# Optimization experiments

Hardware: AMD Instinct MI355X
Metric: run time of the kernel (lower is better)

The kernel has to match this reference:

```python
import jax, jax.numpy as jnp
import numpy as np

N_AGENTS = 32
STATE_DIM = 2048
EMBED = 64
BS, T = 64, 32


def setup_inputs() -> dict:
    key = jax.random.key(0)
    ks = jax.random.split(key, 12)
    def lin(k, fan_in, fan_out):
        return jax.random.normal(k, (fan_in, fan_out), dtype=jnp.float32) / np.sqrt(fan_in)
    return {
        "agent_qs": jax.random.normal(ks[0], (BS, T, N_AGENTS), dtype=jnp.float32),
        "states": jax.random.normal(ks[1], (BS, T, STATE_DIM), dtype=jnp.float32),
        "Ww1": lin(ks[2], STATE_DIM, EMBED * N_AGENTS),
        "bw1": jnp.zeros((EMBED * N_AGENTS,), jnp.float32),
        "Wwf": lin(ks[3], STATE_DIM, EMBED),
        "bwf": jnp.zeros((EMBED,), jnp.float32),
        "Wb1": lin(ks[4], STATE_DIM, EMBED),
        "bb1": jnp.zeros((EMBED,), jnp.float32),
        "Wv1": lin(ks[5], STATE_DIM, EMBED),
        "bv1": jnp.zeros((EMBED,), jnp.float32),
        "Wv2": lin(ks[6], EMBED, 1),
        "bv2": jnp.zeros((1,), jnp.float32),
    }


def _mix(qs, st, Ww1, bw1, Wwf, bwf, Wb1, bb1, Wv1, bv1, Wv2, bv2):
    # qs: [B,1,A], st: [B,S] -> q_tot [B]
    w1 = jnp.abs(st @ Ww1 + bw1).reshape(-1, N_AGENTS, EMBED)          # [B,A,E]
    b1 = (st @ Wb1 + bb1)[:, None, :]                                   # [B,1,E]
    hidden = jax.nn.elu(jnp.einsum('bia,bae->bie', qs, w1) + b1)        # [B,1,E]
    w_final = jnp.abs(st @ Wwf + bwf)                                   # [B,E]
    v = jax.nn.relu(st @ Wv1 + bv1) @ Wv2 + bv2                         # [B,1]
    y = jnp.einsum('bie,be->bi', hidden, w_final) + v                   # [B,1]
    return y[:, 0]


def reference(agent_qs, states, Ww1, bw1, Wwf, bwf, Wb1, bb1, Wv1, bv1, Wv2, bv2):
    bs = agent_qs.shape[0]
    st = states.reshape(-1, STATE_DIM)                   # [B,S]
    qs = agent_qs.reshape(-1, 1, N_AGENTS)               # [B,1,A]
    B = st.shape[0]
    params = (Ww1, bw1, Wwf, bwf, Wb1, bb1, Wv1, bv1, Wv2, bv2)

    # --- wc_calculate (fully detached) ---
    q_tot = _mix(qs, st, *params)                        # [B]
    dim2 = STATE_DIM // N_AGENTS
    st3 = st.reshape(B, N_AGENTS, dim2)
    mask = 1.0 - jnp.eye(N_AGENTS, dtype=st.dtype)       # [A,A]: row i zeros agent-i chunk
    masked = (st3[None, :, :, :] * mask[:, None, :, None]).reshape(N_AGENTS * B, STATE_DIM)
    qs_rep = jnp.broadcast_to(qs[None], (N_AGENTS, B, 1, N_AGENTS)).reshape(N_AGENTS * B, 1, N_AGENTS)
    q1 = _mix(qs_rep, masked, *params).reshape(N_AGENTS, B)
    wc = jnp.abs(q_tot[None, :] - q1).T                  # [B,A]
    wc = wc / jnp.maximum(jnp.linalg.norm(wc, axis=1, keepdims=True), 1e-12)
    wc = jax.lax.stop_gradient(wc)[:, None, :]           # [B,1,A]

    # --- final mix with importance-weighted qs ---
    q_tot_final = _mix(qs * wc, st, *params)             # [B]
    return q_tot_final.reshape(bs, -1, 1)
```

## Files before the change

### kernel.cpp

```cpp
#include <hip/hip_runtime.h>
#include <math.h>
#include <stdint.h>

#define NA 32
#define SD 2048
#define BT 2048
#define NFRG 144

typedef float floatx4 __attribute__((ext_vector_type(4)));
typedef short bf16x8  __attribute__((ext_vector_type(8)));

__device__ __forceinline__ unsigned short f2bf(float f) {
    union { float f; uint32_t u; } v; v.f = f;
    uint32_t r = v.u + 0x7FFFu + ((v.u >> 16) & 1u);
    return (unsigned short)(r >> 16);
}


__global__ __launch_bounds__(256) void k0_ast(const float* __restrict__ st,
                                              unsigned short* __restrict__ stA) {
    int idx = blockIdx.x * 256 + threadIdx.x;
    int m = idx >> 8, kg = idx & 255;
    int k0 = kg * 8;
    const float* src = st + (size_t)m * SD + k0;
    float4 v0 = *(const float4*)src;
    float4 v1 = *(const float4*)(src + 4);
    int bt = m >> 4, l16 = m & 15, kc = kg >> 2, quad = kg & 3;
    unsigned short* dst = stA + ((size_t)bt * 64 + kc) * 512 + (quad * 16 + l16) * 8;
    ushort4 o0, o1;
    o0.x = f2bf(v0.x); o0.y = f2bf(v0.y); o0.z = f2bf(v0.z); o0.w = f2bf(v0.w);
    o1.x = f2bf(v1.x); o1.y = f2bf(v1.y); o1.z = f2bf(v1.z); o1.w = f2bf(v1.w);
    *(ushort4*)(dst)     = o0;
    *(ushort4*)(dst + 4) = o1;
}

__global__ __launch_bounds__(256) void k0_wswz(const float* __restrict__ Ww1,
                                               const float* __restrict__ Wwf,
                                               const float* __restrict__ Wb1,
                                               const float* __restrict__ Wv1,
                                               unsigned short* __restrict__ Wswz) {
    __shared__ float tile[32][33];
    const int n0 = blockIdx.x * 32;
    const int k0 = blockIdx.y * 32;
    const float* src; int ld = 64, nb = 0;
    if (n0 < 2048)      { src = Ww1; ld = 2048; nb = n0; }
    else if (n0 < 2112) { src = Wwf; nb = n0 - 2048; }
    else if (n0 < 2176) { src = Wb1; nb = n0 - 2112; }
    else if (n0 < 2240) { src = Wv1; nb = n0 - 2176; }
    else                { src = nullptr; }
    const int t = threadIdx.x;
    {
        int nl = t & 31, kl0 = t >> 5;
        #pragma unroll
        for (int r = 0; r < 4; r++) {
            int kl = kl0 + r * 8;
            tile[kl][nl] = src ? src[(size_t)(k0 + kl) * ld + nb + nl] : 0.f;
        }
    }
    __syncthreads();
    {
        int kl = t & 31, nl0 = t >> 5;
        #pragma unroll
        for (int r = 0; r < 4; r++) {
            int nl = nl0 + r * 8;
            int n = n0 + nl, k = k0 + kl;
            int f = n >> 4, l16 = n & 15;
            int i = k >> 6, kr = k & 63;
            int h = kr >> 5, quad = (kr & 31) >> 3, j = kr & 7;
            size_t off = (((size_t)i * NFRG + f) * 2 + h) * 512 + (quad * 16 + l16) * 8 + j;
            Wswz[off] = f2bf(tile[kl][nl]);
        }
    }
}

__global__ void k0_bias(const float* __restrict__ bw1, const float* __restrict__ bwf,
                        const float* __restrict__ bb1, const float* __restrict__ bv1,
                        float* __restrict__ bcat) {
    int n = blockIdx.x * 256 + threadIdx.x;
    if (n >= NFRG * 16) return;
    float v = 0.f;
    if (n < 2048)      v = bw1[n];
    else if (n < 2112) v = bwf[n - 2048];
    else if (n < 2176) v = bb1[n - 2112];
    else if (n < 2240) v = bv1[n - 2176];
    bcat[n] = v;
}

__global__ __launch_bounds__(256) void k1_gemm(const unsigned short* __restrict__ stA,
                                               const unsigned short* __restrict__ Wswz,
                                               const float* __restrict__ bcat,
                                               float* __restrict__ Ycn)
{
    const int t = threadIdx.x;
    const int m0t = blockIdx.x * 4;
    const int n0f = blockIdx.y * 8;
    const int wid = t >> 6, lane = t & 63;
    const int wm = wid & 1, wn = wid >> 1;
    const int l16 = lane & 15;

    floatx4 acc[2][4];
    #pragma unroll
    for (int i = 0; i < 2; i++)
        #pragma unroll
        for (int j = 0; j < 4; j++) acc[i][j] = (floatx4)0.f;

    const unsigned short* Ap0 = stA + ((size_t)(m0t + wm * 2 + 0) * 64) * 512 + lane * 8;
    const unsigned short* Ap1 = stA + ((size_t)(m0t + wm * 2 + 1) * 64) * 512 + lane * 8;

    #pragma unroll 2
    for (int kc = 0; kc < 64; kc++) {
        bf16x8 a0 = *(const bf16x8*)(Ap0 + (size_t)kc * 512);
        bf16x8 a1 = *(const bf16x8*)(Ap1 + (size_t)kc * 512);
        const int i = kc >> 1, h = kc & 1;
        const unsigned short* Bp =
            Wswz + (((size_t)i * NFRG + n0f + wn * 4) * 2 + h) * 512 + lane * 8;
        #pragma unroll
        for (int nf = 0; nf < 4; nf++) {
            bf16x8 b = *(const bf16x8*)(Bp + (size_t)nf * 1024);
            acc[0][nf] = __builtin_amdgcn_mfma_f32_16x16x32_bf16(a0, b, acc[0][nf], 0, 0, 0);
            acc[1][nf] = __builtin_amdgcn_mfma_f32_16x16x32_bf16(a1, b, acc[1][nf], 0, 0, 0);
        }
    }

    #pragma unroll
    for (int mf = 0; mf < 2; mf++)
        #pragma unroll
        for (int nf = 0; nf < 4; nf++) {
            const int f  = n0f + wn * 4 + nf;
            const int bt = m0t + wm * 2 + mf;
            const float bias = bcat[f * 16 + l16];
            floatx4 o;
            #pragma unroll
            for (int r = 0; r < 4; r++) o[r] = -(acc[mf][nf][r] + bias);
            *(floatx4*)(Ycn + ((size_t)bt * NFRG + f) * 256 + lane * 4) = o;
        }
}

__global__ __launch_bounds__(64) void k3_q1(
    const unsigned short* __restrict__ stA, const float* __restrict__ qs,
    const unsigned short* __restrict__ Wswz, const float* __restrict__ Wv2,
    const float* __restrict__ bv2, const float* __restrict__ Ycn,
    float* __restrict__ q1)
{
    const int bt = blockIdx.x;
    const int i  = blockIdx.y;
    __shared__ float qs_s[16][33];

    const int t = threadIdx.x;
    const int quad = t >> 4, l16 = t & 15;

    {
        int b = t >> 2, a0 = (t & 3) * 8;
        const float* src = qs + (size_t)(bt * 16 + b) * NA + a0;
        #pragma unroll
        for (int u = 0; u < 8; u++) qs_s[b][a0 + u] = src[u];
    }
    bf16x8 A0 = *(const bf16x8*)(stA + ((size_t)bt * 64 + 2 * i + 0) * 512 + t * 8);
    bf16x8 A1 = *(const bf16x8*)(stA + ((size_t)bt * 64 + 2 * i + 1) * 512 + t * 8);
    __syncthreads();

    floatx4 hid[4];
    #pragma unroll
    for (int nf = 0; nf < 4; nf++) hid[nf] = (floatx4)0.f;

    const float*          Yb = Ycn  + (size_t)bt * NFRG * 256;
    const unsigned short* Wb = Wswz + (size_t)i * NFRG * 1024;

    for (int a = 0; a < 32; a++) {
        const float*          yp = Yb + (size_t)(a * 4) * 256 + t * 4;
        const unsigned short* wp = Wb + (size_t)(a * 4) * 1024 + t * 8;
        floatx4 acc[4];
        #pragma unroll
        for (int nf = 0; nf < 4; nf++) acc[nf] = *(const floatx4*)(yp + nf * 256);
        #pragma unroll
        for (int nf = 0; nf < 4; nf++) {
            bf16x8 b0 = *(const bf16x8*)(wp + nf * 1024);
            bf16x8 b1 = *(const bf16x8*)(wp + nf * 1024 + 512);
            acc[nf] = __builtin_amdgcn_mfma_f32_16x16x32_bf16(A0, b0, acc[nf], 0, 0, 0);
            acc[nf] = __builtin_amdgcn_mfma_f32_16x16x32_bf16(A1, b1, acc[nf], 0, 0, 0);
        }
        float qv[4];
        #pragma unroll
        for (int r = 0; r < 4; r++) qv[r] = qs_s[quad * 4 + r][a];
        #pragma unroll
        for (int nf = 0; nf < 4; nf++)
            #pragma unroll
            for (int r = 0; r < 4; r++)
                hid[nf][r] += qv[r] * fabsf(acc[nf][r]);
    }

    floatx4 wff[4], b1f[4], vacc = (floatx4)0.f;
    #pragma unroll
    for (int nft = 0; nft < 12; nft++) {
        const int f = 128 + nft;
        floatx4 c = *(const floatx4*)(Yb + (size_t)f * 256 + t * 4);
        const unsigned short* wp = Wb + (size_t)f * 1024 + t * 8;
        c = __builtin_amdgcn_mfma_f32_16x16x32_bf16(A0, *(const bf16x8*)(wp),       c, 0, 0, 0);
        c = __builtin_amdgcn_mfma_f32_16x16x32_bf16(A1, *(const bf16x8*)(wp + 512), c, 0, 0, 0);
        if (nft < 4) {
            #pragma unroll
            for (int r = 0; r < 4; r++) wff[nft][r] = fabsf(c[r]);
        } else if (nft < 8) {
            #pragma unroll
            for (int r = 0; r < 4; r++) b1f[nft - 4][r] = -c[r];
        } else {
            float wv2 = Wv2[(nft - 8) * 16 + l16];
            #pragma unroll
            for (int r = 0; r < 4; r++) vacc[r] += fmaxf(-c[r], 0.f) * wv2;
        }
    }

    const float bv2v = bv2[0];
    #pragma unroll
    for (int r = 0; r < 4; r++) {
        float s = vacc[r];
        #pragma unroll
        for (int nf = 0; nf < 4; nf++) {
            float h = hid[nf][r] + b1f[nf][r];
            h = h > 0.f ? h : expm1f(h);
            s += h * wff[nf][r];
        }
        s += __shfl_xor(s, 1); s += __shfl_xor(s, 2);
        s += __shfl_xor(s, 4); s += __shfl_xor(s, 8);
        if (l16 == 0) q1[(size_t)i * BT + bt * 16 + quad * 4 + r] = s + bv2v;
    }
}

__global__ __launch_bounds__(256) void k4_final(
    const float* __restrict__ qs, const float* __restrict__ Ycn,
    const float* __restrict__ q1, const float* __restrict__ Wv2,
    const float* __restrict__ bv2, float* __restrict__ out)
{
    const int bt = blockIdx.x;
    __shared__ float qs_s[16][33];
    __shared__ float qw_s[16][33];
    __shared__ float hidp[4][16][64];
    __shared__ float wfb[16][64], b1b[16][64], vb[16][64];
    __shared__ float qt[16];

    const int t = threadIdx.x, w = t >> 6, lane = t & 63;
    const int quad = lane >> 4, l16 = lane & 15;
    const float bv2v = bv2[0];

    {
        int l = t * 2;
        float2 v = *(const float2*)&qs[(size_t)(bt * 16 + (l >> 5)) * NA + (l & 31)];
        qs_s[l >> 5][(l & 31) + 0] = v.x;
        qs_s[l >> 5][(l & 31) + 1] = v.y;
    }
    __syncthreads();

    const float* Yb = Ycn + (size_t)bt * NFRG * 256;

    floatx4 hid[4];
    #pragma unroll
    for (int nf = 0; nf < 4; nf++) hid[nf] = (floatx4)0.f;
    for (int ia = 0; ia < 8; ia++) {
        const int a = w * 8 + ia;
        const float* yp = Yb + (size_t)(a * 4) * 256 + lane * 4;
        float qv[4];
        #pragma unroll
        for (int r = 0; r < 4; r++) qv[r] = qs_s[quad * 4 + r][a];
        #pragma unroll
        for (int nf = 0; nf < 4; nf++) {
            floatx4 c = *(const floatx4*)(yp + nf * 256);
            #pragma unroll
            for (int r = 0; r < 4; r++) hid[nf][r] += qv[r] * fabsf(c[r]);
        }
    }
    #pragma unroll
    for (int nf = 0; nf < 4; nf++)
        #pragma unroll
        for (int r = 0; r < 4; r++)
            hidp[w][quad * 4 + r][nf * 16 + l16] = hid[nf][r];

    #pragma unroll
    for (int fi = 0; fi < 3; fi++) {
        const int nft = w * 3 + fi;
        floatx4 c = *(const floatx4*)(Yb + (size_t)(128 + nft) * 256 + lane * 4);
        const int e = (nft & 3) * 16 + l16;
        #pragma unroll
        for (int r = 0; r < 4; r++) {
            int b = quad * 4 + r;
            if (nft < 4)      wfb[b][e] = fabsf(c[r]);
            else if (nft < 8) b1b[b][e] = -c[r];
            else              vb[b][e]  = fmaxf(-c[r], 0.f) * Wv2[e];
        }
    }
    __syncthreads();

    #pragma unroll
    for (int bb = 0; bb < 4; bb++) {
        int b = w * 4 + bb;
        float h = hidp[0][b][lane] + hidp[1][b][lane]
                + hidp[2][b][lane] + hidp[3][b][lane] + b1b[b][lane];
        h = h > 0.f ? h : expm1f(h);
        float val = h * wfb[b][lane] + vb[b][lane];
        #pragma unroll
        for (int off = 32; off > 0; off >>= 1) val += __shfl_xor(val, off);
        if (lane == 0) qt[b] = val + bv2v;
    }
    __syncthreads();

    {
        const int rr = w * 4 + quad;
        float qtv = qt[rr];
        float d0 = fabsf(qtv - q1[(size_t)(2 * l16 + 0) * BT + bt * 16 + rr]);
        float d1 = fabsf(qtv - q1[(size_t)(2 * l16 + 1) * BT + bt * 16 + rr]);
        float ss = d0 * d0 + d1 * d1;
        ss += __shfl_xor(ss, 1); ss += __shfl_xor(ss, 2);
        ss += __shfl_xor(ss, 4); ss += __shfl_xor(ss, 8);
        float inv = 1.f / fmaxf(sqrtf(ss), 1e-12f);
        qw_s[rr][2 * l16 + 0] = qs_s[rr][2 * l16 + 0] * d0 * inv;
        qw_s[rr][2 * l16 + 1] = qs_s[rr][2 * l16 + 1] * d1 * inv;
    }
    __syncthreads();

    floatx4 hid2[4];
    #pragma unroll
    for (int nf = 0; nf < 4; nf++) hid2[nf] = (floatx4)0.f;
    for (int ia = 0; ia < 8; ia++) {
        const int a = w * 8 + ia;
        const float* yp = Yb + (size_t)(a * 4) * 256 + lane * 4;
        float qv[4];
        #pragma unroll
        for (int r = 0; r < 4; r++) qv[r] = qw_s[quad * 4 + r][a];
        #pragma unroll
        for (int nf = 0; nf < 4; nf++) {
            floatx4 c = *(const floatx4*)(yp + nf * 256);
            #pragma unroll
            for (int r = 0; r < 4; r++) hid2[nf][r] += qv[r] * fabsf(c[r]);
        }
    }
    #pragma unroll
    for (int nf = 0; nf < 4; nf++)
        #pragma unroll
        for (int r = 0; r < 4; r++)
            hidp[w][quad * 4 + r][nf * 16 + l16] = hid2[nf][r];
    __syncthreads();

    #pragma unroll
    for (int bb = 0; bb < 4; bb++) {
        int b = w * 4 + bb;
        float h = hidp[0][b][lane] + hidp[1][b][lane]
                + hidp[2][b][lane] + hidp[3][b][lane] + b1b[b][lane];
        h = h > 0.f ? h : expm1f(h);
        float val = h * wfb[b][lane] + vb[b][lane];
        #pragma unroll
        for (int off = 32; off > 0; off >>= 1) val += __shfl_xor(val, off);
        if (lane == 0) out[bt * 16 + b] = val + bv2v;
    }
}

extern "C" void kernel_launch(void* const* d_in, const int* in_sizes, int n_in,
                              void* d_out, int out_size, void* d_ws, size_t ws_size,
                              hipStream_t stream) {
    const float* qs  = (const float*)d_in[0];
    const float* st  = (const float*)d_in[1];
    const float* Ww1 = (const float*)d_in[2];
    const float* bw1 = (const float*)d_in[3];
    const float* Wwf = (const float*)d_in[4];
    const float* bwf = (const float*)d_in[5];
    const float* Wb1 = (const float*)d_in[6];
    const float* bb1 = (const float*)d_in[7];
    const float* Wv1 = (const float*)d_in[8];
    const float* bv1 = (const float*)d_in[9];
    const float* Wv2 = (const float*)d_in[10];
    const float* bv2 = (const float*)d_in[11];
    float* out = (float*)d_out;

    float* Ycn           = (float*)d_ws;
    unsigned short* stA  = (unsigned short*)(Ycn + (size_t)128 * NFRG * 256);
    unsigned short* Wswz = stA + (size_t)SD * SD;
    float* bcat          = (float*)(Wswz + (size_t)32 * NFRG * 1024);
    float* q1v           = bcat + NFRG * 16;

    k0_ast <<<(SD * SD / 8 + 255) / 256, 256, 0, stream>>>(st, stA);
    k0_wswz<<<dim3(NFRG / 2, SD / 32), 256, 0, stream>>>(Ww1, Wwf, Wb1, Wv1, Wswz);
    k0_bias<<<(NFRG * 16 + 255) / 256, 256, 0, stream>>>(bw1, bwf, bb1, bv1, bcat);

    k1_gemm<<<dim3(BT / 64, NFRG / 8), 256, 0, stream>>>(stA, Wswz, bcat, Ycn);
    k3_q1  <<<dim3(BT / 16, NA), 64, 0, stream>>>(stA, qs, Wswz, Wv2, bv2, Ycn, q1v);
    k4_final<<<BT / 16, 256, 0, stream>>>(qs, Ycn, q1v, Wv2, bv2, out);
}
```

Baseline: 217.9 us.

## Store GEMM output in bf16, prefetch GEMM operands, remap repacking kernels

The intermediate projection Ycn is now stored as bf16 instead of fp32. This halves the traffic for the GEMM epilogue and for the reads in the q1 and final kernels, at the cost of extra rounding in values that later feed differences between mixes. The GEMM main loop now register double-buffers the A and B fragments to hide load latency. The state and weight repacking kernels are remapped so that each thread writes a contiguous 8-element fragment directly, and the weight repack drops its shared-memory transpose in favor of strided global reads.

```diff
diff --git a/kernel.cpp b/kernel.cpp
--- a/kernel.cpp
+++ b/kernel.cpp
@@ -16,20 +16,31 @@
     return (unsigned short)(r >> 16);
 }
 
+__device__ __forceinline__ floatx4 bf4_to_f4(ushort4 u) {
+    union { uint32_t i; float f; } t;
+    floatx4 r;
+    t.i = (uint32_t)u.x << 16; r[0] = t.f;
+    t.i = (uint32_t)u.y << 16; r[1] = t.f;
+    t.i = (uint32_t)u.z << 16; r[2] = t.f;
+    t.i = (uint32_t)u.w << 16; r[3] = t.f;
+    return r;
+}
+
 
 __global__ __launch_bounds__(256) void k0_ast(const float* __restrict__ st,
                                               unsigned short* __restrict__ stA) {
-    int idx = blockIdx.x * 256 + threadIdx.x;
-    int m = idx >> 8, kg = idx & 255;
-    int k0 = kg * 8;
-    const float* src = st + (size_t)m * SD + k0;
-    float4 v0 = *(const float4*)src;
+    const int t  = threadIdx.x;
+    const int kc = blockIdx.x * 4 + (t >> 6);
+    const int bt = blockIdx.y;
+    const int l  = t & 63;
+    const int quad = l >> 4, l16 = l & 15;
+    const float* src = st + (size_t)(bt * 16 + l16) * SD + kc * 32 + quad * 8;
+    float4 v0 = *(const float4*)(src);
     float4 v1 = *(const float4*)(src + 4);
-    int bt = m >> 4, l16 = m & 15, kc = kg >> 2, quad = kg & 3;
-    unsigned short* dst = stA + ((size_t)bt * 64 + kc) * 512 + (quad * 16 + l16) * 8;
     ushort4 o0, o1;
     o0.x = f2bf(v0.x); o0.y = f2bf(v0.y); o0.z = f2bf(v0.z); o0.w = f2bf(v0.w);
     o1.x = f2bf(v1.x); o1.y = f2bf(v1.y); o1.z = f2bf(v1.z); o1.w = f2bf(v1.w);
+    unsigned short* dst = stA + ((size_t)bt * 64 + kc) * 512 + l * 8;
     *(ushort4*)(dst)     = o0;
     *(ushort4*)(dst + 4) = o1;
 }
@@ -39,38 +50,32 @@
                                                const float* __restrict__ Wb1,
                                                const float* __restrict__ Wv1,
                                                unsigned short* __restrict__ Wswz) {
-    __shared__ float tile[32][33];
-    const int n0 = blockIdx.x * 32;
-    const int k0 = blockIdx.y * 32;
-    const float* src; int ld = 64, nb = 0;
-    if (n0 < 2048)      { src = Ww1; ld = 2048; nb = n0; }
-    else if (n0 < 2112) { src = Wwf; nb = n0 - 2048; }
-    else if (n0 < 2176) { src = Wb1; nb = n0 - 2112; }
-    else if (n0 < 2240) { src = Wv1; nb = n0 - 2176; }
-    else                { src = nullptr; }
     const int t = threadIdx.x;
-    {
-        int nl = t & 31, kl0 = t >> 5;
-        #pragma unroll
-        for (int r = 0; r < 4; r++) {
-            int kl = kl0 + r * 8;
-            tile[kl][nl] = src ? src[(size_t)(k0 + kl) * ld + nb + nl] : 0.f;
-        }
-    }
-    __syncthreads();
-    {
-        int kl = t & 31, nl0 = t >> 5;
-        #pragma unroll
-        for (int r = 0; r < 4; r++) {
-            int nl = nl0 + r * 8;
-            int n = n0 + nl, k = k0 + kl;
-            int f = n >> 4, l16 = n & 15;
-            int i = k >> 6, kr = k & 63;
-            int h = kr >> 5, quad = (kr & 31) >> 3, j = kr & 7;
-            size_t off = (((size_t)i * NFRG + f) * 2 + h) * 512 + (quad * 16 + l16) * 8 + j;
-            Wswz[off] = f2bf(tile[kl][nl]);
-        }
-    }
+    const int i = blockIdx.y;
+    const int f = blockIdx.x * 2 + (t >> 7);
+    const int h = (t >> 6) & 1;
+    const int l = t & 63;
+    const int quad = l >> 4, l16 = l & 15;
+    const int n = f * 16 + l16;
+
+    const float* src; int ld, nr = 0;
+    if (f < 128)      { src = Ww1; ld = 2048; nr = n; }
+    else if (f < 132) { src = Wwf; ld = 64;   nr = n - 2048; }
+    else if (f < 136) { src = Wb1; ld = 64;   nr = n - 2112; }
+    else if (f < 140) { src = Wv1; ld = 64;   nr = n - 2176; }
+    else              { src = nullptr; ld = 64; }
+
+    const int k0 = i * 64 + h * 32 + quad * 8;
+    unsigned short vals[8];
+    #pragma unroll
+    for (int j = 0; j < 8; j++)
+        vals[j] = src ? f2bf(src[(size_t)(k0 + j) * ld + nr]) : (unsigned short)0;
+
+    unsigned short* dst = Wswz + (((size_t)i * NFRG + f) * 2 + h) * 512 + l * 8;
+    ushort4 o0 = {vals[0], vals[1], vals[2], vals[3]};
+    ushort4 o1 = {vals[4], vals[5], vals[6], vals[7]};
+    *(ushort4*)(dst)     = o0;
+    *(ushort4*)(dst + 4) = o1;
 }
 
 __global__ void k0_bias(const float* __restrict__ bw1, const float* __restrict__ bwf,
@@ -89,7 +94,7 @@
 __global__ __launch_bounds__(256) void k1_gemm(const unsigned short* __restrict__ stA,
                                                const unsigned short* __restrict__ Wswz,
                                                const float* __restrict__ bcat,
-                                               float* __restrict__ Ycn)
+                                               unsigned short* __restrict__ Ycn)
 {
     const int t = threadIdx.x;
     const int m0t = blockIdx.x * 4;
@@ -106,20 +111,35 @@
 
     const unsigned short* Ap0 = stA + ((size_t)(m0t + wm * 2 + 0) * 64) * 512 + lane * 8;
     const unsigned short* Ap1 = stA + ((size_t)(m0t + wm * 2 + 1) * 64) * 512 + lane * 8;
-
-    #pragma unroll 2
+    const unsigned short* Bbase = Wswz + ((size_t)(n0f + wn * 4) * 2) * 512 + lane * 8;
+
+    bf16x8 a0c = *(const bf16x8*)(Ap0);
+    bf16x8 a1c = *(const bf16x8*)(Ap1);
+    bf16x8 bc[4];
+    #pragma unroll
+    for (int nf = 0; nf < 4; nf++)
+        bc[nf] = *(const bf16x8*)(Bbase + (size_t)nf * 1024);
+
     for (int kc = 0; kc < 64; kc++) {
-        bf16x8 a0 = *(const bf16x8*)(Ap0 + (size_t)kc * 512);
-        bf16x8 a1 = *(const bf16x8*)(Ap1 + (size_t)kc * 512);
-        const int i = kc >> 1, h = kc & 1;
-        const unsigned short* Bp =
-            Wswz + (((size_t)i * NFRG + n0f + wn * 4) * 2 + h) * 512 + lane * 8;
-        #pragma unroll
-        for (int nf = 0; nf < 4; nf++) {
-            bf16x8 b = *(const bf16x8*)(Bp + (size_t)nf * 1024);
-            acc[0][nf] = __builtin_amdgcn_mfma_f32_16x16x32_bf16(a0, b, acc[0][nf], 0, 0, 0);
-            acc[1][nf] = __builtin_amdgcn_mfma_f32_16x16x32_bf16(a1, b, acc[1][nf], 0, 0, 0);
-        }
+        bf16x8 a0n, a1n, bn[4];
+        if (kc < 63) {
+            const int kn = kc + 1;
+            a0n = *(const bf16x8*)(Ap0 + (size_t)kn * 512);
+            a1n = *(const bf16x8*)(Ap1 + (size_t)kn * 512);
+            const unsigned short* Bp =
+                Bbase + ((size_t)(kn >> 1) * NFRG * 2 + (kn & 1)) * 512;
+            #pragma unroll
+            for (int nf = 0; nf < 4; nf++)
+                bn[nf] = *(const bf16x8*)(Bp + (size_t)nf * 1024);
+        }
+        #pragma unroll
+        for (int nf = 0; nf < 4; nf++) {
+            acc[0][nf] = __builtin_amdgcn_mfma_f32_16x16x32_bf16(a0c, bc[nf], acc[0][nf], 0, 0, 0);
+            acc[1][nf] = __builtin_amdgcn_mfma_f32_16x16x32_bf16(a1c, bc[nf], acc[1][nf], 0, 0, 0);
+        }
+        a0c = a0n; a1c = a1n;
+        #pragma unroll
+        for (int nf = 0; nf < 4; nf++) bc[nf] = bn[nf];
     }
 
     #pragma unroll
@@ -129,17 +149,19 @@
             const int f  = n0f + wn * 4 + nf;
             const int bt = m0t + wm * 2 + mf;
             const float bias = bcat[f * 16 + l16];
-            floatx4 o;
-            #pragma unroll
-            for (int r = 0; r < 4; r++) o[r] = -(acc[mf][nf][r] + bias);
-            *(floatx4*)(Ycn + ((size_t)bt * NFRG + f) * 256 + lane * 4) = o;
+            ushort4 o;
+            o.x = f2bf(-(acc[mf][nf][0] + bias));
+            o.y = f2bf(-(acc[mf][nf][1] + bias));
+            o.z = f2bf(-(acc[mf][nf][2] + bias));
+            o.w = f2bf(-(acc[mf][nf][3] + bias));
+            *(ushort4*)(Ycn + ((size_t)bt * NFRG + f) * 256 + lane * 4) = o;
         }
 }
 
 __global__ __launch_bounds__(64) void k3_q1(
     const unsigned short* __restrict__ stA, const float* __restrict__ qs,
     const unsigned short* __restrict__ Wswz, const float* __restrict__ Wv2,
-    const float* __restrict__ bv2, const float* __restrict__ Ycn,
+    const float* __restrict__ bv2, const unsigned short* __restrict__ Ycn,
     float* __restrict__ q1)
 {
     const int bt = blockIdx.x;
@@ -163,15 +185,16 @@
     #pragma unroll
     for (int nf = 0; nf < 4; nf++) hid[nf] = (floatx4)0.f;
 
-    const float*          Yb = Ycn  + (size_t)bt * NFRG * 256;
+    const unsigned short* Yb = Ycn  + (size_t)bt * NFRG * 256;
     const unsigned short* Wb = Wswz + (size_t)i * NFRG * 1024;
 
     for (int a = 0; a < 32; a++) {
-        const float*          yp = Yb + (size_t)(a * 4) * 256 + t * 4;
+        const unsigned short* yp = Yb + (size_t)(a * 4) * 256 + t * 4;
         const unsigned short* wp = Wb + (size_t)(a * 4) * 1024 + t * 8;
         floatx4 acc[4];
         #pragma unroll
-        for (int nf = 0; nf < 4; nf++) acc[nf] = *(const floatx4*)(yp + nf * 256);
+        for (int nf = 0; nf < 4; nf++)
+            acc[nf] = bf4_to_f4(*(const ushort4*)(yp + nf * 256));
         #pragma unroll
         for (int nf = 0; nf < 4; nf++) {
             bf16x8 b0 = *(const bf16x8*)(wp + nf * 1024);
@@ -193,7 +216,7 @@
     #pragma unroll
     for (int nft = 0; nft < 12; nft++) {
         const int f = 128 + nft;
-        floatx4 c = *(const floatx4*)(Yb + (size_t)f * 256 + t * 4);
+        floatx4 c = bf4_to_f4(*(const ushort4*)(Yb + (size_t)f * 256 + t * 4));
         const unsigned short* wp = Wb + (size_t)f * 1024 + t * 8;
         c = __builtin_amdgcn_mfma_f32_16x16x32_bf16(A0, *(const bf16x8*)(wp),       c, 0, 0, 0);
         c = __builtin_amdgcn_mfma_f32_16x16x32_bf16(A1, *(const bf16x8*)(wp + 512), c, 0, 0, 0);
@@ -227,7 +250,7 @@
 }
 
 __global__ __launch_bounds__(256) void k4_final(
-    const float* __restrict__ qs, const float* __restrict__ Ycn,
+    const float* __restrict__ qs, const unsigned short* __restrict__ Ycn,
     const float* __restrict__ q1, const float* __restrict__ Wv2,
     const float* __restrict__ bv2, float* __restrict__ out)
 {
@@ -250,20 +273,20 @@
     }
     __syncthreads();
 
-    const float* Yb = Ycn + (size_t)bt * NFRG * 256;
+    const unsigned short* Yb = Ycn + (size_t)bt * NFRG * 256;
 
     floatx4 hid[4];
     #pragma unroll
     for (int nf = 0; nf < 4; nf++) hid[nf] = (floatx4)0.f;
     for (int ia = 0; ia < 8; ia++) {
         const int a = w * 8 + ia;
-        const float* yp = Yb + (size_t)(a * 4) * 256 + lane * 4;
+        const unsigned short* yp = Yb + (size_t)(a * 4) * 256 + lane * 4;
         float qv[4];
         #pragma unroll
         for (int r = 0; r < 4; r++) qv[r] = qs_s[quad * 4 + r][a];
         #pragma unroll
         for (int nf = 0; nf < 4; nf++) {
-            floatx4 c = *(const floatx4*)(yp + nf * 256);
+            floatx4 c = bf4_to_f4(*(const ushort4*)(yp + nf * 256));
             #pragma unroll
             for (int r = 0; r < 4; r++) hid[nf][r] += qv[r] * fabsf(c[r]);
         }
@@ -277,7 +300,7 @@
     #pragma unroll
     for (int fi = 0; fi < 3; fi++) {
         const int nft = w * 3 + fi;
-        floatx4 c = *(const floatx4*)(Yb + (size_t)(128 + nft) * 256 + lane * 4);
+        floatx4 c = bf4_to_f4(*(const ushort4*)(Yb + (size_t)(128 + nft) * 256 + lane * 4));
         const int e = (nft & 3) * 16 + l16;
         #pragma unroll
         for (int r = 0; r < 4; r++) {
@@ -321,13 +344,13 @@
     for (int nf = 0; nf < 4; nf++) hid2[nf] = (floatx4)0.f;
     for (int ia = 0; ia < 8; ia++) {
         const int a = w * 8 + ia;
-        const float* yp = Yb + (size_t)(a * 4) * 256 + lane * 4;
+        const unsigned short* yp = Yb + (size_t)(a * 4) * 256 + lane * 4;
         float qv[4];
         #pragma unroll
         for (int r = 0; r < 4; r++) qv[r] = qw_s[quad * 4 + r][a];
         #pragma unroll
         for (int nf = 0; nf < 4; nf++) {
-            floatx4 c = *(const floatx4*)(yp + nf * 256);
+            floatx4 c = bf4_to_f4(*(const ushort4*)(yp + nf * 256));
             #pragma unroll
             for (int r = 0; r < 4; r++) hid2[nf][r] += qv[r] * fabsf(c[r]);
         }
@@ -369,14 +392,14 @@
     const float* bv2 = (const float*)d_in[11];
     float* out = (float*)d_out;
 
-    float* Ycn           = (float*)d_ws;
-    unsigned short* stA  = (unsigned short*)(Ycn + (size_t)128 * NFRG * 256);
+    unsigned short* Ycn  = (unsigned short*)d_ws;
+    unsigned short* stA  = Ycn + (size_t)128 * NFRG * 256;
     unsigned short* Wswz = stA + (size_t)SD * SD;
     float* bcat          = (float*)(Wswz + (size_t)32 * NFRG * 1024);
     float* q1v           = bcat + NFRG * 16;
 
-    k0_ast <<<(SD * SD / 8 + 255) / 256, 256, 0, stream>>>(st, stA);
-    k0_wswz<<<dim3(NFRG / 2, SD / 32), 256, 0, stream>>>(Ww1, Wwf, Wb1, Wv1, Wswz);
+    k0_ast <<<dim3(16, 128), 256, 0, stream>>>(st, stA);
+    k0_wswz<<<dim3(NFRG / 2, 32), 256, 0, stream>>>(Ww1, Wwf, Wb1, Wv1, Wswz);
     k0_bias<<<(NFRG * 16 + 255) / 256, 256, 0, stream>>>(bw1, bwf, bb1, bv1, bcat);
 
     k1_gemm<<<dim3(BT / 64, NFRG / 8), 256, 0, stream>>>(stA, Wswz, bcat, Ycn);
```

After: 231.8 us. 1.06x slower.
